# Performance work log

Hardware: AMD Instinct MI355X
Metric: run time of the kernel (lower is better)

The kernel has to match this reference:

```python
import jax, jax.numpy as jnp
import numpy as np

N = 512
H = 128
L = 4
NUM_RBF = 50
CUTOFF = 5.0
NMOL = 16
OUT = 1


def setup_inputs() -> dict:
    key = jax.random.key(0)
    ks = jax.random.split(key, 12)
    s = lambda f: 1.0 / np.sqrt(f)
    atomic_numbers = jax.random.randint(ks[0], (N,), 0, 100)
    positions = jax.random.normal(ks[1], (N, 3), dtype=jnp.float32) * 2.0
    batch = jnp.sort(jax.random.randint(ks[2], (N,), 0, NMOL))
    return {
        'atomic_numbers': atomic_numbers,
        'positions': positions,
        'batch': batch,
        'embed': jax.random.normal(ks[3], (100, H), dtype=jnp.float32) * 0.1,
        'msg_w1': jax.random.normal(ks[4], (L, H + NUM_RBF + 3, H), dtype=jnp.float32) * s(H + NUM_RBF + 3),
        'msg_b1': jnp.zeros((L, H), jnp.float32),
        'msg_w2': jax.random.normal(ks[5], (L, H, H), dtype=jnp.float32) * s(H),
        'msg_b2': jnp.zeros((L, H), jnp.float32),
        'upd_w1': jax.random.normal(ks[6], (L, 2 * H, H), dtype=jnp.float32) * s(2 * H),
        'upd_b1': jnp.zeros((L, H), jnp.float32),
        'upd_w2': jax.random.normal(ks[7], (L, H, H), dtype=jnp.float32) * s(H),
        'upd_b2': jnp.zeros((L, H), jnp.float32),
        'out_w1': jax.random.normal(ks[8], (H, H // 2), dtype=jnp.float32) * s(H),
        'out_b1': jnp.zeros((H // 2,), jnp.float32),
        'out_w2': jax.random.normal(ks[9], (H // 2, OUT), dtype=jnp.float32) * s(H // 2),
        'out_b2': jnp.zeros((OUT,), jnp.float32),
    }


def _forward(atomic_numbers, positions, batch, embed, msg_w1, msg_b1, msg_w2,
             msg_b2, upd_w1, upd_b1, upd_w2, upd_b2, out_w1, out_b1, out_w2, out_b2):
    x = embed[jnp.clip(atomic_numbers, 0, 99)]                      # [N,H]
    # all-pairs geometry: row i = source, col j = target (matches repeat_interleave/repeat)
    diff = positions[:, None, :] - positions[None, :, :]            # [N,N,3]
    dist = jnp.linalg.norm(diff, axis=-1)                           # [N,N]
    not_self = jnp.arange(N)[:, None] != jnp.arange(N)[None, :]
    valid = (dist < CUTOFF) & not_self                              # [N,N] edge mask
    dirs = diff / jnp.maximum(dist, 1e-8)[..., None]                # [N,N,3]
    # gaussian RBF: centers linspace(0, cutoff, num_rbf), width = cutoff/num_rbf
    centers = jnp.linspace(0.0, CUTOFF, NUM_RBF)
    width = CUTOFF / NUM_RBF
    rbf = jnp.exp(-(dist[..., None] - centers) ** 2 / (2.0 * width ** 2))  # [N,N,50]

    for l in range(L):
        # Linear over concat([x_j, rbf, dirs]) split by input blocks (same math)
        Wx = msg_w1[l, :H]
        Wr = msg_w1[l, H:H + NUM_RBF]
        Wd = msg_w1[l, H + NUM_RBF:]
        pre = (x @ Wx)[:, None, :] \
            + jnp.einsum('ijr,rh->ijh', rbf, Wr) \
            + jnp.einsum('ijd,dh->ijh', dirs, Wd) + msg_b1[l]       # [N,N,H]
        m = jax.nn.silu(pre) @ msg_w2[l] + msg_b2[l]                # [N,N,H]
        m = jnp.where(valid[..., None], m, 0.0)
        aggr = m.sum(axis=0)                                        # scatter-add to target j
        upd_in = jnp.concatenate([x, aggr], axis=-1)                # [N,2H]
        x = x + jax.nn.silu(upd_in @ upd_w1[l] + upd_b1[l]) @ upd_w2[l] + upd_b2[l]

    # per-molecule mean pool
    sums = jax.ops.segment_sum(x, batch, num_segments=NMOL)         # [NMOL,H]
    counts = jax.ops.segment_sum(jnp.ones((N,), x.dtype), batch, num_segments=NMOL)
    pooled = sums / jnp.maximum(counts, 1.0)[:, None]
    return jax.nn.silu(pooled @ out_w1 + out_b1) @ out_w2 + out_b2  # [NMOL,OUT]


def reference(atomic_numbers, positions, batch, embed, msg_w1, msg_b1, msg_w2,
              msg_b2, upd_w1, upd_b1, upd_w2, upd_b2, out_w1, out_b1, out_w2, out_b2):
    return _forward(atomic_numbers, positions, batch, embed, msg_w1, msg_b1, msg_w2,
                    msg_b2, upd_w1, upd_b1, upd_w2, upd_b2, out_w1, out_b1, out_w2, out_b2)
```

## Files before the change

### kernel.cpp

```cpp
#include <hip/hip_runtime.h>
#include <math.h>

#define N 512
#define H 128
#define L 4
#define NUM_RBF 50
#define NMOL 16
#define SUPER 64
#define MAXS 8

typedef __attribute__((ext_vector_type(8))) short short8;
typedef __attribute__((ext_vector_type(4))) float float4v;
typedef __attribute__((ext_vector_type(4))) int int4v;

__device__ __forceinline__ float silu_f(float v) {
    return v / (1.0f + __expf(-v));
}

__device__ __forceinline__ unsigned short f2bf(float f) {
    unsigned int u = __float_as_uint(f);
    unsigned int r = (u + 0x7FFFu + ((u >> 16) & 1u)) >> 16;
    return (unsigned short)r;
}

__device__ __forceinline__ void gld_lds16(const void* g, void* l) {
    __builtin_amdgcn_global_load_lds(
        (const __attribute__((address_space(1))) unsigned int*)g,
        (__attribute__((address_space(3))) unsigned int*)l, 16, 0, 0);
}

__global__ __launch_bounds__(512) void k_embed_lin(const int* __restrict__ an,
                                                   const float* __restrict__ embed,
                                                   const float* __restrict__ pos,
                                                   const float* __restrict__ wx,
                                                   const float* __restrict__ b1,
                                                   float* __restrict__ x,
                                                   float* __restrict__ a,
                                                   int* __restrict__ nbr,
                                                   int* __restrict__ ncnt,
                                                   unsigned short* __restrict__ Fg) {
    int j = blockIdx.x;
    int tid = threadIdx.x;
    int lane = tid & 63;
    int wave = tid >> 6;
    int h = tid & 127;
    int grp = tid >> 7;

    __shared__ float xs[H];
    __shared__ int wsum8[8];
    __shared__ float part[4][H];

    float pjx = pos[j * 3 + 0], pjy = pos[j * 3 + 1], pjz = pos[j * 3 + 2];

    if (tid < H) {
        int z = an[j];
        z = min(max(z, 0), 99);
        float xv = embed[z * H + tid];
        xs[tid] = xv;
        x[j * H + tid] = xv;
    }

    int padded;
    {
        int i = tid;
        float dx = pos[i * 3 + 0] - pjx;
        float dy = pos[i * 3 + 1] - pjy;
        float dz = pos[i * 3 + 2] - pjz;
        float d2 = dx * dx + dy * dy + dz * dz;
        int valid = (d2 < 25.0f) && (i != j);
        unsigned long long m = __ballot(valid);
        int pre = __popcll(m & ((1ull << lane) - 1ull));
        if (lane == 0) wsum8[wave] = __popcll(m);
        __syncthreads();
        int wbase = 0, total = 0;
        for (int w = 0; w < 8; w++) {
            if (w < wave) wbase += wsum8[w];
            total += wsum8[w];
        }
        if (valid) nbr[j * 512 + wbase + pre] = i;
        padded = (total + 63) & ~63;
        for (int s = total + tid; s < padded; s += 512) nbr[j * 512 + s] = j;
        if (tid == 0) ncnt[j] = total;
    }

    {
        float p0 = 0.f, p1 = 0.f, p2 = 0.f, p3 = 0.f;
        int k0 = grp * 32;
#pragma unroll 8
        for (int k = 0; k < 32; k += 4) {
            p0 += xs[k0 + k]     * wx[(k0 + k)     * H + h];
            p1 += xs[k0 + k + 1] * wx[(k0 + k + 1) * H + h];
            p2 += xs[k0 + k + 2] * wx[(k0 + k + 2) * H + h];
            p3 += xs[k0 + k + 3] * wx[(k0 + k + 3) * H + h];
        }
        part[grp][h] = (p0 + p1) + (p2 + p3);
    }
    __syncthreads();
    if (grp == 0)
        a[j * H + h] = part[0][h] + part[1][h] + part[2][h] + part[3][h] + b1[h];

    const float DELTA = 5.0f / 49.0f;
    int kb = (tid & 3) * 16;
#pragma unroll
    for (int pass = 0; pass < 4; pass++) {
        int slot = pass * 128 + (tid >> 2);
        if (slot < padded) {
            int ni = nbr[j * 512 + slot];
            float dx = pos[ni * 3 + 0] - pjx;
            float dy = pos[ni * 3 + 1] - pjy;
            float dz = pos[ni * 3 + 2] - pjz;
            float d = sqrtf(dx * dx + dy * dy + dz * dz);
            float rinv = 1.0f / fmaxf(d, 1e-8f);
            unsigned short vals[16];
#pragma unroll
            for (int qq = 0; qq < 16; qq++) {
                int k = kb + qq;
                float v;
                if (k < NUM_RBF) {
                    float tt = d - (float)k * DELTA;
                    v = __expf(-50.0f * tt * tt);
                } else if (k == NUM_RBF)     v = dx * rinv;
                else if (k == NUM_RBF + 1)   v = dy * rinv;
                else if (k == NUM_RBF + 2)   v = dz * rinv;
                else                         v = 0.0f;
                vals[qq] = f2bf(v);
            }
            int row = slot & 63;
            unsigned short* tile = Fg + (((size_t)(j * MAXS + (slot >> 6))) << 12);
            int c0 = kb >> 3;
            int4v p0, p1;
#pragma unroll
            for (int q = 0; q < 4; q++) {
                p0[q] = (int)((unsigned)vals[2 * q]     | ((unsigned)vals[2 * q + 1] << 16));
                p1[q] = (int)((unsigned)vals[8 + 2 * q] | ((unsigned)vals[9 + 2 * q] << 16));
            }
            *(int4v*)(tile + row * 64 + (((c0    ) ^ (row & 7)) << 3)) = p0;
            *(int4v*)(tile + row * 64 + (((c0 + 1) ^ (row & 7)) << 3)) = p1;
        }
    }
}

__global__ __launch_bounds__(512) void k_layer(const float* __restrict__ a,
                                               const int* __restrict__ nbr,
                                               const int* __restrict__ ncnt,
                                               const unsigned short* __restrict__ Fg,
                                               const float* __restrict__ wfeat,
                                               const float* __restrict__ w2,
                                               const float* __restrict__ b2,
                                               const float* __restrict__ u1,
                                               const float* __restrict__ ub1,
                                               const float* __restrict__ u2,
                                               const float* __restrict__ ub2,
                                               float* __restrict__ x,
                                               const float* __restrict__ wxn,
                                               const float* __restrict__ b1n,
                                               float* __restrict__ a_next) {
    int j = blockIdx.x;
    int tid = threadIdx.x;
    int g = tid >> 8;
    int lane = tid & 63;
    int wv4 = (tid >> 6) & 3;
    int nn = lane & 15;
    int quad = lane >> 4;
    int hbase = wv4 * 32;

    __shared__ __align__(16) unsigned short F[2][2][SUPER * 64];
    __shared__ __align__(16) int nidx_all[512];
    __shared__ float sjp[2][H];
    __shared__ float sj[H], xj[H], ag[H], hid[H], xn[H];
    __shared__ float part[4][H];

    int cnt = ncnt[j];

    if (tid < 2 * H) sjp[tid >> 7][tid & 127] = 0.0f;
    if (tid < H) xj[tid] = x[j * H + tid];
    nidx_all[tid] = nbr[j * 512 + tid];

    short8 bfrag[2][2];
    for (int c = 0; c < 2; c++) {
        for (int t = 0; t < 2; t++) {
            short8 b;
            int h = hbase + 16 * t + nn;
#pragma unroll
            for (int jj = 0; jj < 8; jj++) {
                int k = c * 32 + quad * 8 + jj;
                float v = (k < NUM_RBF + 3) ? wfeat[k * H + h] : 0.0f;
                b[jj] = (short)f2bf(v);
            }
            bfrag[c][t] = b;
        }
    }

    int S = (cnt + 63) >> 6;
    int rounds = (S + 1) >> 1;

    auto stage_tile = [&](int s, int b) {
        const char* src = (const char*)(Fg + (((size_t)(j * MAXS + s)) << 12));
        char* dst = (char*)&F[g][b][0];
#pragma unroll
        for (int q = 0; q < 2; q++) {
            int off = (wv4 + 4 * q) << 10;
            gld_lds16(src + off + lane * 16, dst + off);
        }
    };

    if (g < S) stage_tile(g, 0);
    __syncthreads();

    float pacc0 = 0.0f, pacc1 = 0.0f;

    for (int r = 0; r < rounds; r++) {
        int s = 2 * r + g;
        int sn = 2 * (r + 1) + g;
        if (sn < S) stage_tile(sn, (r + 1) & 1);
        if (s < S) {
            int cur = r & 1;
#pragma unroll
            for (int it = 0; it < SUPER / 16; it++) {
                int lbase = it * 16 + quad * 4;
                int4v ni4 = *(const int4v*)&nidx_all[s * 64 + lbase];
                float av0[4], av1[4];
#pragma unroll
                for (int rr = 0; rr < 4; rr++) {
                    av0[rr] = a[ni4[rr] * H + hbase + nn];
                    av1[rr] = a[ni4[rr] * H + hbase + 16 + nn];
                }
                int row = it * 16 + nn;
                const char* fb = (const char*)&F[g][cur][0] + row * 128;
                short8 afrag0 = *(const short8*)(fb + ((quad       ^ (row & 7)) << 4));
                short8 afrag1 = *(const short8*)(fb + (((quad + 4) ^ (row & 7)) << 4));
                float4v acc0 = {0.0f, 0.0f, 0.0f, 0.0f};
                float4v acc1 = {0.0f, 0.0f, 0.0f, 0.0f};
                acc0 = __builtin_amdgcn_mfma_f32_16x16x32_bf16(afrag0, bfrag[0][0], acc0, 0, 0, 0);
                acc0 = __builtin_amdgcn_mfma_f32_16x16x32_bf16(afrag1, bfrag[1][0], acc0, 0, 0, 0);
                acc1 = __builtin_amdgcn_mfma_f32_16x16x32_bf16(afrag0, bfrag[0][1], acc1, 0, 0, 0);
                acc1 = __builtin_amdgcn_mfma_f32_16x16x32_bf16(afrag1, bfrag[1][1], acc1, 0, 0, 0);
#pragma unroll
                for (int rr = 0; rr < 4; rr++) {
                    float vm = (s * 64 + lbase + rr < cnt) ? 1.0f : 0.0f;
                    pacc0 += vm * silu_f(acc0[rr] + av0[rr]);
                    pacc1 += vm * silu_f(acc1[rr] + av1[rr]);
                }
            }
        }
        __syncthreads();
    }

    pacc0 += __shfl_xor(pacc0, 16, 64);
    pacc0 += __shfl_xor(pacc0, 32, 64);
    pacc1 += __shfl_xor(pacc1, 16, 64);
    pacc1 += __shfl_xor(pacc1, 32, 64);
    if (lane < 16) {
        sjp[g][hbase + lane]      = pacc0;
        sjp[g][hbase + 16 + lane] = pacc1;
    }
    __syncthreads();
    if (tid < H) sj[tid] = sjp[0][tid] + sjp[1][tid];
    __syncthreads();

    int h = tid & 127;
    int grp = tid >> 7;

    {
        float p0 = 0.f, p1 = 0.f, p2 = 0.f, p3 = 0.f;
        int k0 = grp * 32;
#pragma unroll 8
        for (int k = 0; k < 32; k += 4) {
            p0 += sj[k0 + k]     * w2[(k0 + k)     * H + h];
            p1 += sj[k0 + k + 1] * w2[(k0 + k + 1) * H + h];
            p2 += sj[k0 + k + 2] * w2[(k0 + k + 2) * H + h];
            p3 += sj[k0 + k + 3] * w2[(k0 + k + 3) * H + h];
        }
        part[grp][h] = (p0 + p1) + (p2 + p3);
    }
    __syncthreads();
    if (grp == 0) ag[h] = part[0][h] + part[1][h] + part[2][h] + part[3][h] + (float)cnt * b2[h];
    __syncthreads();

    {
        const float* src = (grp < 2) ? xj : ag;
        int sbase = (grp & 1) * 64;
        int k0 = grp * 64;
        float p0 = 0.f, p1 = 0.f, p2 = 0.f, p3 = 0.f;
#pragma unroll 8
        for (int k = 0; k < 64; k += 4) {
            p0 += src[sbase + k]     * u1[(k0 + k)     * H + h];
            p1 += src[sbase + k + 1] * u1[(k0 + k + 1) * H + h];
            p2 += src[sbase + k + 2] * u1[(k0 + k + 2) * H + h];
            p3 += src[sbase + k + 3] * u1[(k0 + k + 3) * H + h];
        }
        part[grp][h] = (p0 + p1) + (p2 + p3);
    }
    __syncthreads();
    if (grp == 0) hid[h] = silu_f(part[0][h] + part[1][h] + part[2][h] + part[3][h] + ub1[h]);
    __syncthreads();

    {
        float p0 = 0.f, p1 = 0.f, p2 = 0.f, p3 = 0.f;
        int k0 = grp * 32;
#pragma unroll 8
        for (int k = 0; k < 32; k += 4) {
            p0 += hid[k0 + k]     * u2[(k0 + k)     * H + h];
            p1 += hid[k0 + k + 1] * u2[(k0 + k + 1) * H + h];
            p2 += hid[k0 + k + 2] * u2[(k0 + k + 2) * H + h];
            p3 += hid[k0 + k + 3] * u2[(k0 + k + 3) * H + h];
        }
        part[grp][h] = (p0 + p1) + (p2 + p3);
    }
    __syncthreads();
    if (grp == 0) {
        float xv = xj[h] + part[0][h] + part[1][h] + part[2][h] + part[3][h] + ub2[h];
        x[j * H + h] = xv;
        xn[h] = xv;
    }

    if (a_next != nullptr) {
        __syncthreads();
        float p0 = 0.f, p1 = 0.f, p2 = 0.f, p3 = 0.f;
        int k0 = grp * 32;
#pragma unroll 8
        for (int k = 0; k < 32; k += 4) {
            p0 += xn[k0 + k]     * wxn[(k0 + k)     * H + h];
            p1 += xn[k0 + k + 1] * wxn[(k0 + k + 1) * H + h];
            p2 += xn[k0 + k + 2] * wxn[(k0 + k + 2) * H + h];
            p3 += xn[k0 + k + 3] * wxn[(k0 + k + 3) * H + h];
        }
        part[grp][h] = (p0 + p1) + (p2 + p3);
        __syncthreads();
        if (grp == 0)
            a_next[j * H + h] = part[0][h] + part[1][h] + part[2][h] + part[3][h] + b1n[h];
    }
}

__global__ __launch_bounds__(512) void k_pool(const float* __restrict__ x,
                                              const int* __restrict__ batch,
                                              const float* __restrict__ ow1,
                                              const float* __restrict__ ob1,
                                              const float* __restrict__ ow2,
                                              const float* __restrict__ ob2,
                                              float* __restrict__ out) {
    int m = blockIdx.x;
    int tid = threadIdx.x;
    int h = tid & 127;
    int q = tid >> 7;
    __shared__ int lo_s, hi_s;
    __shared__ float psum[4][H];
    __shared__ float pooled[H];
    __shared__ float hid[H / 2];

    if (tid == 0) {
        int a = 0, b = N;
        while (a < b) { int mid = (a + b) >> 1; if (batch[mid] < m) a = mid + 1; else b = mid; }
        lo_s = a;
        b = N;
        while (a < b) { int mid = (a + b) >> 1; if (batch[mid] < m + 1) a = mid + 1; else b = mid; }
        hi_s = a;
    }
    __syncthreads();

    int lo = lo_s, hi = hi_s;
    float s = 0.0f;
    for (int i = lo + q; i < hi; i += 4) s += x[i * H + h];
    psum[q][h] = s;
    __syncthreads();
    if (q == 0) pooled[h] = (psum[0][h] + psum[1][h] + psum[2][h] + psum[3][h]) / (float)max(hi - lo, 1);
    __syncthreads();

    if (tid < H / 2) {
        float p0 = 0.f, p1 = 0.f;
        for (int k = 0; k < H; k += 2) {
            p0 += pooled[k]     * ow1[(k)     * (H / 2) + h];
            p1 += pooled[k + 1] * ow1[(k + 1) * (H / 2) + h];
        }
        hid[h] = silu_f(p0 + p1 + ob1[h]);
    }
    __syncthreads();

    if (tid == 0) {
        float o = ob2[0];
        for (int k = 0; k < H / 2; k++) o += hid[k] * ow2[k];
        out[m] = o;
    }
}

extern "C" void kernel_launch(void* const* d_in, const int* in_sizes, int n_in,
                              void* d_out, int out_size, void* d_ws, size_t ws_size,
                              hipStream_t stream) {
    const int*   an      = (const int*)d_in[0];
    const float* pos     = (const float*)d_in[1];
    const int*   batch   = (const int*)d_in[2];
    const float* embed   = (const float*)d_in[3];
    const float* msg_w1  = (const float*)d_in[4];
    const float* msg_b1  = (const float*)d_in[5];
    const float* msg_w2  = (const float*)d_in[6];
    const float* msg_b2  = (const float*)d_in[7];
    const float* upd_w1  = (const float*)d_in[8];
    const float* upd_b1  = (const float*)d_in[9];
    const float* upd_w2  = (const float*)d_in[10];
    const float* upd_b2  = (const float*)d_in[11];
    const float* out_w1  = (const float*)d_in[12];
    const float* out_b1  = (const float*)d_in[13];
    const float* out_w2  = (const float*)d_in[14];
    const float* out_b2  = (const float*)d_in[15];
    float* out = (float*)d_out;

    float* x    = (float*)d_ws;
    float* a0   = x + N * H;
    float* a1   = a0 + N * H;
    int*   nbr  = (int*)(a1 + N * H);
    int*   ncnt = nbr + N * 512;
    unsigned short* Fg = (unsigned short*)(ncnt + N);

    const int W1ROWS = H + NUM_RBF + 3;

    k_embed_lin<<<N, 512, 0, stream>>>(an, embed, pos, msg_w1, msg_b1, x, a0, nbr, ncnt, Fg);
    for (int l = 0; l < L; l++) {
        float* a_cur  = (l & 1) ? a1 : a0;
        float* a_next = (l + 1 < L) ? ((l & 1) ? a0 : a1) : nullptr;
        const float* wxn = (l + 1 < L) ? (msg_w1 + (l + 1) * W1ROWS * H) : nullptr;
        const float* b1n = (l + 1 < L) ? (msg_b1 + (l + 1) * H) : nullptr;
        k_layer<<<N, 512, 0, stream>>>(a_cur, nbr, ncnt, Fg,
                                       msg_w1 + l * W1ROWS * H + H * H,
                                       msg_w2 + l * H * H, msg_b2 + l * H,
                                       upd_w1 + l * 2 * H * H, upd_b1 + l * H,
                                       upd_w2 + l * H * H, upd_b2 + l * H,
                                       x, wxn, b1n, a_next);
    }
    k_pool<<<NMOL, 512, 0, stream>>>(x, batch, out_w1, out_b1, out_w2, out_b2, out);
}
```

Measured before the change: 215.8 us.

## Split layer kernel into message and batched 4-node update kernels

The fused per-node layer kernel is split into k_msg, which computes each node's summed message activation and writes it to a global buffer, and k_upd, which runs the dense update MLP for four nodes per block. In k_upd each weight load is reused across four rows, and the per-block partial-sum reductions with their extra barriers go away. In exchange each layer now launches twice and makes an extra global round trip for the intermediate sums, and the update kernel runs only 128 blocks.

```diff
diff --git a/kernel.cpp b/kernel.cpp
--- a/kernel.cpp
+++ b/kernel.cpp
@@ -140,21 +140,12 @@
     }
 }
 
-__global__ __launch_bounds__(512) void k_layer(const float* __restrict__ a,
-                                               const int* __restrict__ nbr,
-                                               const int* __restrict__ ncnt,
-                                               const unsigned short* __restrict__ Fg,
-                                               const float* __restrict__ wfeat,
-                                               const float* __restrict__ w2,
-                                               const float* __restrict__ b2,
-                                               const float* __restrict__ u1,
-                                               const float* __restrict__ ub1,
-                                               const float* __restrict__ u2,
-                                               const float* __restrict__ ub2,
-                                               float* __restrict__ x,
-                                               const float* __restrict__ wxn,
-                                               const float* __restrict__ b1n,
-                                               float* __restrict__ a_next) {
+__global__ __launch_bounds__(512) void k_msg(const float* __restrict__ a,
+                                             const int* __restrict__ nbr,
+                                             const int* __restrict__ ncnt,
+                                             const unsigned short* __restrict__ Fg,
+                                             const float* __restrict__ wfeat,
+                                             float* __restrict__ sjg) {
     int j = blockIdx.x;
     int tid = threadIdx.x;
     int g = tid >> 8;
@@ -167,13 +158,8 @@
     __shared__ __align__(16) unsigned short F[2][2][SUPER * 64];
     __shared__ __align__(16) int nidx_all[512];
     __shared__ float sjp[2][H];
-    __shared__ float sj[H], xj[H], ag[H], hid[H], xn[H];
-    __shared__ float part[4][H];
 
     int cnt = ncnt[j];
-
-    if (tid < 2 * H) sjp[tid >> 7][tid & 127] = 0.0f;
-    if (tid < H) xj[tid] = x[j * H + tid];
     nidx_all[tid] = nbr[j * 512 + tid];
 
     short8 bfrag[2][2];
@@ -255,80 +241,92 @@
         sjp[g][hbase + 16 + lane] = pacc1;
     }
     __syncthreads();
-    if (tid < H) sj[tid] = sjp[0][tid] + sjp[1][tid];
-    __syncthreads();
-
+    if (tid < H) sjg[j * H + tid] = sjp[0][tid] + sjp[1][tid];
+}
+
+__global__ __launch_bounds__(512) void k_upd(const float* __restrict__ sjg,
+                                             const int* __restrict__ ncnt,
+                                             const float* __restrict__ w2,
+                                             const float* __restrict__ b2,
+                                             const float* __restrict__ u1,
+                                             const float* __restrict__ ub1,
+                                             const float* __restrict__ u2,
+                                             const float* __restrict__ ub2,
+                                             float* __restrict__ x,
+                                             const float* __restrict__ wxn,
+                                             const float* __restrict__ b1n,
+                                             float* __restrict__ a_next) {
+    int j0 = blockIdx.x * 4;
+    int tid = threadIdx.x;
     int h = tid & 127;
-    int grp = tid >> 7;
+    int r = tid >> 7;
+
+    __shared__ float sj[4][H], xj[4][H], ag[4][H], hid[4][H], xn[4][H];
+    __shared__ float cntv[4];
+
+    sj[r][h] = sjg[(j0 + r) * H + h];
+    xj[r][h] = x[(j0 + r) * H + h];
+    if (tid < 4) cntv[tid] = (float)ncnt[j0 + tid];
+    __syncthreads();
 
     {
         float p0 = 0.f, p1 = 0.f, p2 = 0.f, p3 = 0.f;
-        int k0 = grp * 32;
-#pragma unroll 8
-        for (int k = 0; k < 32; k += 4) {
-            p0 += sj[k0 + k]     * w2[(k0 + k)     * H + h];
-            p1 += sj[k0 + k + 1] * w2[(k0 + k + 1) * H + h];
-            p2 += sj[k0 + k + 2] * w2[(k0 + k + 2) * H + h];
-            p3 += sj[k0 + k + 3] * w2[(k0 + k + 3) * H + h];
-        }
-        part[grp][h] = (p0 + p1) + (p2 + p3);
-    }
-    __syncthreads();
-    if (grp == 0) ag[h] = part[0][h] + part[1][h] + part[2][h] + part[3][h] + (float)cnt * b2[h];
-    __syncthreads();
-
-    {
-        const float* src = (grp < 2) ? xj : ag;
-        int sbase = (grp & 1) * 64;
-        int k0 = grp * 64;
-        float p0 = 0.f, p1 = 0.f, p2 = 0.f, p3 = 0.f;
-#pragma unroll 8
-        for (int k = 0; k < 64; k += 4) {
-            p0 += src[sbase + k]     * u1[(k0 + k)     * H + h];
-            p1 += src[sbase + k + 1] * u1[(k0 + k + 1) * H + h];
-            p2 += src[sbase + k + 2] * u1[(k0 + k + 2) * H + h];
-            p3 += src[sbase + k + 3] * u1[(k0 + k + 3) * H + h];
-        }
-        part[grp][h] = (p0 + p1) + (p2 + p3);
-    }
-    __syncthreads();
-    if (grp == 0) hid[h] = silu_f(part[0][h] + part[1][h] + part[2][h] + part[3][h] + ub1[h]);
+#pragma unroll 8
+        for (int k = 0; k < H; k += 4) {
+            p0 += sj[r][k]     * w2[(k)     * H + h];
+            p1 += sj[r][k + 1] * w2[(k + 1) * H + h];
+            p2 += sj[r][k + 2] * w2[(k + 2) * H + h];
+            p3 += sj[r][k + 3] * w2[(k + 3) * H + h];
+        }
+        ag[r][h] = (p0 + p1) + (p2 + p3) + cntv[r] * b2[h];
+    }
     __syncthreads();
 
     {
         float p0 = 0.f, p1 = 0.f, p2 = 0.f, p3 = 0.f;
-        int k0 = grp * 32;
-#pragma unroll 8
-        for (int k = 0; k < 32; k += 4) {
-            p0 += hid[k0 + k]     * u2[(k0 + k)     * H + h];
-            p1 += hid[k0 + k + 1] * u2[(k0 + k + 1) * H + h];
-            p2 += hid[k0 + k + 2] * u2[(k0 + k + 2) * H + h];
-            p3 += hid[k0 + k + 3] * u2[(k0 + k + 3) * H + h];
-        }
-        part[grp][h] = (p0 + p1) + (p2 + p3);
-    }
-    __syncthreads();
-    if (grp == 0) {
-        float xv = xj[h] + part[0][h] + part[1][h] + part[2][h] + part[3][h] + ub2[h];
-        x[j * H + h] = xv;
-        xn[h] = xv;
+#pragma unroll 8
+        for (int k = 0; k < H; k += 4) {
+            p0 += xj[r][k]     * u1[(k)     * H + h];
+            p1 += xj[r][k + 1] * u1[(k + 1) * H + h];
+            p2 += xj[r][k + 2] * u1[(k + 2) * H + h];
+            p3 += xj[r][k + 3] * u1[(k + 3) * H + h];
+        }
+#pragma unroll 8
+        for (int k = 0; k < H; k += 4) {
+            p0 += ag[r][k]     * u1[(H + k)     * H + h];
+            p1 += ag[r][k + 1] * u1[(H + k + 1) * H + h];
+            p2 += ag[r][k + 2] * u1[(H + k + 2) * H + h];
+            p3 += ag[r][k + 3] * u1[(H + k + 3) * H + h];
+        }
+        hid[r][h] = silu_f((p0 + p1) + (p2 + p3) + ub1[h]);
+    }
+    __syncthreads();
+
+    {
+        float p0 = 0.f, p1 = 0.f, p2 = 0.f, p3 = 0.f;
+#pragma unroll 8
+        for (int k = 0; k < H; k += 4) {
+            p0 += hid[r][k]     * u2[(k)     * H + h];
+            p1 += hid[r][k + 1] * u2[(k + 1) * H + h];
+            p2 += hid[r][k + 2] * u2[(k + 2) * H + h];
+            p3 += hid[r][k + 3] * u2[(k + 3) * H + h];
+        }
+        float xv = xj[r][h] + (p0 + p1) + (p2 + p3) + ub2[h];
+        x[(j0 + r) * H + h] = xv;
+        xn[r][h] = xv;
     }
 
     if (a_next != nullptr) {
         __syncthreads();
         float p0 = 0.f, p1 = 0.f, p2 = 0.f, p3 = 0.f;
-        int k0 = grp * 32;
-#pragma unroll 8
-        for (int k = 0; k < 32; k += 4) {
-            p0 += xn[k0 + k]     * wxn[(k0 + k)     * H + h];
-            p1 += xn[k0 + k + 1] * wxn[(k0 + k + 1) * H + h];
-            p2 += xn[k0 + k + 2] * wxn[(k0 + k + 2) * H + h];
-            p3 += xn[k0 + k + 3] * wxn[(k0 + k + 3) * H + h];
-        }
-        part[grp][h] = (p0 + p1) + (p2 + p3);
-        __syncthreads();
-        if (grp == 0)
-            a_next[j * H + h] = part[0][h] + part[1][h] + part[2][h] + part[3][h] + b1n[h];
+#pragma unroll 8
+        for (int k = 0; k < H; k += 4) {
+            p0 += xn[r][k]     * wxn[(k)     * H + h];
+            p1 += xn[r][k + 1] * wxn[(k + 1) * H + h];
+            p2 += xn[r][k + 2] * wxn[(k + 2) * H + h];
+            p3 += xn[r][k + 3] * wxn[(k + 3) * H + h];
+        }
+        a_next[(j0 + r) * H + h] = (p0 + p1) + (p2 + p3) + b1n[h];
     }
 }
 
@@ -407,7 +405,8 @@
     float* x    = (float*)d_ws;
     float* a0   = x + N * H;
     float* a1   = a0 + N * H;
-    int*   nbr  = (int*)(a1 + N * H);
+    float* sjg  = a1 + N * H;
+    int*   nbr  = (int*)(sjg + N * H);
     int*   ncnt = nbr + N * 512;
     unsigned short* Fg = (unsigned short*)(ncnt + N);
 
@@ -419,12 +418,13 @@
         float* a_next = (l + 1 < L) ? ((l & 1) ? a0 : a1) : nullptr;
         const float* wxn = (l + 1 < L) ? (msg_w1 + (l + 1) * W1ROWS * H) : nullptr;
         const float* b1n = (l + 1 < L) ? (msg_b1 + (l + 1) * H) : nullptr;
-        k_layer<<<N, 512, 0, stream>>>(a_cur, nbr, ncnt, Fg,
-                                       msg_w1 + l * W1ROWS * H + H * H,
-                                       msg_w2 + l * H * H, msg_b2 + l * H,
-                                       upd_w1 + l * 2 * H * H, upd_b1 + l * H,
-                                       upd_w2 + l * H * H, upd_b2 + l * H,
-                                       x, wxn, b1n, a_next);
+        k_msg<<<N, 512, 0, stream>>>(a_cur, nbr, ncnt, Fg,
+                                     msg_w1 + l * W1ROWS * H + H * H, sjg);
+        k_upd<<<N / 4, 512, 0, stream>>>(sjg, ncnt,
+                                         msg_w2 + l * H * H, msg_b2 + l * H,
+                                         upd_w1 + l * 2 * H * H, upd_b1 + l * H,
+                                         upd_w2 + l * H * H, upd_b2 + l * H,
+                                         x, wxn, b1n, a_next);
     }
     k_pool<<<NMOL, 512, 0, stream>>>(x, batch, out_w1, out_b1, out_w2, out_b2, out);
 }
```

Result: slower. 245.5 us (+13.8%).

## Fuse all layers into one persistent cooperative kernel with grid syncs

Applied to the files above, without the earlier changes.

Replaces the six separate launches (embed, four layers, pool) with a single cooperative kernel of 256 blocks. Each block owns two nodes for the whole run and keeps their x state, neighbour lists and counts in shared memory. Layers are separated by grid.sync(), which removes per-launch overhead and the global round-trips for x, nbr and ncnt. In exchange, each block does twice the serial work with half the blocks, and every layer waits on a grid-wide barrier.

```diff
diff --git a/kernel.cpp b/kernel.cpp
--- a/kernel.cpp
+++ b/kernel.cpp
@@ -1,5 +1,8 @@
 #include <hip/hip_runtime.h>
+#include <hip/hip_cooperative_groups.h>
 #include <math.h>
+
+namespace cg = cooperative_groups;
 
 #define N 512
 #define H 128
@@ -8,6 +11,7 @@
 #define NMOL 16
 #define SUPER 64
 #define MAXS 8
+#define NB 256
 
 typedef __attribute__((ext_vector_type(8))) short short8;
 typedef __attribute__((ext_vector_type(4))) float float4v;
@@ -29,363 +33,357 @@
         (__attribute__((address_space(3))) unsigned int*)l, 16, 0, 0);
 }
 
-__global__ __launch_bounds__(512) void k_embed_lin(const int* __restrict__ an,
-                                                   const float* __restrict__ embed,
-                                                   const float* __restrict__ pos,
-                                                   const float* __restrict__ wx,
-                                                   const float* __restrict__ b1,
-                                                   float* __restrict__ x,
-                                                   float* __restrict__ a,
-                                                   int* __restrict__ nbr,
-                                                   int* __restrict__ ncnt,
-                                                   unsigned short* __restrict__ Fg) {
-    int j = blockIdx.x;
-    int tid = threadIdx.x;
-    int lane = tid & 63;
-    int wave = tid >> 6;
-    int h = tid & 127;
-    int grp = tid >> 7;
-
-    __shared__ float xs[H];
+__global__ __launch_bounds__(512) void k_all(
+    const int* __restrict__ an, const float* __restrict__ pos,
+    const int* __restrict__ batch, const float* __restrict__ embed,
+    const float* __restrict__ msg_w1, const float* __restrict__ msg_b1,
+    const float* __restrict__ msg_w2, const float* __restrict__ msg_b2,
+    const float* __restrict__ upd_w1, const float* __restrict__ upd_b1,
+    const float* __restrict__ upd_w2, const float* __restrict__ upd_b2,
+    const float* __restrict__ ow1, const float* __restrict__ ob1,
+    const float* __restrict__ ow2, const float* __restrict__ ob2,
+    float* __restrict__ out,
+    float* __restrict__ xg, float* __restrict__ a0g, float* __restrict__ a1g,
+    unsigned short* __restrict__ Fg)
+{
+    cg::grid_group grid = cg::this_grid();
+    const int bid = blockIdx.x;
+    const int tid = threadIdx.x;
+    const int lane = tid & 63;
+    const int wave = tid >> 6;
+    const int h128 = tid & 127;
+    const int grp = tid >> 7;
+    const int g = tid >> 8;
+    const int wv4 = (tid >> 6) & 3;
+    const int nn = lane & 15;
+    const int quad = lane >> 4;
+    const int hbase = wv4 * 32;
+
+    __shared__ __align__(16) unsigned short F[2][2][SUPER * 64];
+    __shared__ __align__(16) int nidx[2][512];
+    __shared__ float xcur[2][H];
+    __shared__ float sjv[2][H], sjp[2][H];
+    __shared__ float tp[4][H];
+    __shared__ float agv[2][H], hidv[2][H];
     __shared__ int wsum8[8];
-    __shared__ float part[4][H];
-
-    float pjx = pos[j * 3 + 0], pjy = pos[j * 3 + 1], pjz = pos[j * 3 + 2];
-
-    if (tid < H) {
-        int z = an[j];
-        z = min(max(z, 0), 99);
-        float xv = embed[z * H + tid];
-        xs[tid] = xv;
-        x[j * H + tid] = xv;
+    __shared__ int cnt_s[2];
+    __shared__ int lo_s, hi_s;
+
+    for (int n = 0; n < 2; n++) {
+        const int j = bid + n * NB;
+        const float pjx = pos[j * 3 + 0], pjy = pos[j * 3 + 1], pjz = pos[j * 3 + 2];
+
+        if (tid < H) {
+            int z = an[j];
+            z = min(max(z, 0), 99);
+            xcur[n][tid] = embed[z * H + tid];
+        }
+
+        int padded;
+        {
+            int i = tid;
+            float dx = pos[i * 3 + 0] - pjx;
+            float dy = pos[i * 3 + 1] - pjy;
+            float dz = pos[i * 3 + 2] - pjz;
+            float d2 = dx * dx + dy * dy + dz * dz;
+            int valid = (d2 < 25.0f) && (i != j);
+            unsigned long long m = __ballot(valid);
+            int pre = __popcll(m & ((1ull << lane) - 1ull));
+            if (lane == 0) wsum8[wave] = __popcll(m);
+            __syncthreads();
+            int wbase = 0, total = 0;
+            for (int w = 0; w < 8; w++) {
+                if (w < wave) wbase += wsum8[w];
+                total += wsum8[w];
+            }
+            if (valid) nidx[n][wbase + pre] = i;
+            padded = (total + 63) & ~63;
+            for (int s = total + tid; s < padded; s += 512) nidx[n][s] = j;
+            if (tid == 0) cnt_s[n] = total;
+        }
+
+        {
+            float p0 = 0.f, p1 = 0.f, p2 = 0.f, p3 = 0.f;
+            int k0 = grp * 32;
+#pragma unroll 8
+            for (int k = 0; k < 32; k += 4) {
+                p0 += xcur[n][k0 + k]     * msg_w1[(k0 + k)     * H + h128];
+                p1 += xcur[n][k0 + k + 1] * msg_w1[(k0 + k + 1) * H + h128];
+                p2 += xcur[n][k0 + k + 2] * msg_w1[(k0 + k + 2) * H + h128];
+                p3 += xcur[n][k0 + k + 3] * msg_w1[(k0 + k + 3) * H + h128];
+            }
+            tp[grp][h128] = (p0 + p1) + (p2 + p3);
+        }
+        __syncthreads();
+        if (grp == 0)
+            a0g[j * H + h128] = tp[0][h128] + tp[1][h128] + tp[2][h128] + tp[3][h128] + msg_b1[h128];
+
+        {
+            const float DELTA = 5.0f / 49.0f;
+            int kb = (tid & 3) * 16;
+#pragma unroll
+            for (int pass = 0; pass < 4; pass++) {
+                int slot = pass * 128 + (tid >> 2);
+                if (slot < padded) {
+                    int ni = nidx[n][slot];
+                    float dx = pos[ni * 3 + 0] - pjx;
+                    float dy = pos[ni * 3 + 1] - pjy;
+                    float dz = pos[ni * 3 + 2] - pjz;
+                    float d = sqrtf(dx * dx + dy * dy + dz * dz);
+                    float rinv = 1.0f / fmaxf(d, 1e-8f);
+                    unsigned short vals[16];
+#pragma unroll
+                    for (int qq = 0; qq < 16; qq++) {
+                        int k = kb + qq;
+                        float v;
+                        if (k < NUM_RBF) {
+                            float tt = d - (float)k * DELTA;
+                            v = __expf(-50.0f * tt * tt);
+                        } else if (k == NUM_RBF)     v = dx * rinv;
+                        else if (k == NUM_RBF + 1)   v = dy * rinv;
+                        else if (k == NUM_RBF + 2)   v = dz * rinv;
+                        else                         v = 0.0f;
+                        vals[qq] = f2bf(v);
+                    }
+                    int row = slot & 63;
+                    unsigned short* tile = Fg + (((size_t)(j * MAXS + (slot >> 6))) << 12);
+                    int c0 = kb >> 3;
+                    int4v p0, p1;
+#pragma unroll
+                    for (int q = 0; q < 4; q++) {
+                        p0[q] = (int)((unsigned)vals[2 * q]     | ((unsigned)vals[2 * q + 1] << 16));
+                        p1[q] = (int)((unsigned)vals[8 + 2 * q] | ((unsigned)vals[9 + 2 * q] << 16));
+                    }
+                    *(int4v*)(tile + row * 64 + (((c0    ) ^ (row & 7)) << 3)) = p0;
+                    *(int4v*)(tile + row * 64 + (((c0 + 1) ^ (row & 7)) << 3)) = p1;
+                }
+            }
+        }
+        __syncthreads();
     }
-
-    int padded;
-    {
-        int i = tid;
-        float dx = pos[i * 3 + 0] - pjx;
-        float dy = pos[i * 3 + 1] - pjy;
-        float dz = pos[i * 3 + 2] - pjz;
-        float d2 = dx * dx + dy * dy + dz * dz;
-        int valid = (d2 < 25.0f) && (i != j);
-        unsigned long long m = __ballot(valid);
-        int pre = __popcll(m & ((1ull << lane) - 1ull));
-        if (lane == 0) wsum8[wave] = __popcll(m);
-        __syncthreads();
-        int wbase = 0, total = 0;
-        for (int w = 0; w < 8; w++) {
-            if (w < wave) wbase += wsum8[w];
-            total += wsum8[w];
-        }
-        if (valid) nbr[j * 512 + wbase + pre] = i;
-        padded = (total + 63) & ~63;
-        for (int s = total + tid; s < padded; s += 512) nbr[j * 512 + s] = j;
-        if (tid == 0) ncnt[j] = total;
+    grid.sync();
+
+    const int W1R = H + NUM_RBF + 3;
+    for (int l = 0; l < L; l++) {
+        const float* wfeat = msg_w1 + l * W1R * H + H * H;
+        const float* w2  = msg_w2 + l * H * H;
+        const float* b2  = msg_b2 + l * H;
+        const float* u1  = upd_w1 + l * 2 * H * H;
+        const float* ub1 = upd_b1 + l * H;
+        const float* u2  = upd_w2 + l * H * H;
+        const float* ub2 = upd_b2 + l * H;
+        const float* acur = (l & 1) ? a1g : a0g;
+        float* anext = (l & 1) ? a0g : a1g;
+        const float* wxn = msg_w1 + (l + 1) * W1R * H;
+        const float* b1n = msg_b1 + (l + 1) * H;
+
+        short8 bfrag[2][2];
+        for (int c = 0; c < 2; c++) {
+            for (int t = 0; t < 2; t++) {
+                short8 b;
+                int hh = hbase + 16 * t + nn;
+#pragma unroll
+                for (int jj = 0; jj < 8; jj++) {
+                    int k = c * 32 + quad * 8 + jj;
+                    float v = (k < NUM_RBF + 3) ? wfeat[k * H + hh] : 0.0f;
+                    b[jj] = (short)f2bf(v);
+                }
+                bfrag[c][t] = b;
+            }
+        }
+
+        for (int n = 0; n < 2; n++) {
+            const int j = bid + n * NB;
+            int cnt = cnt_s[n];
+            int S = (cnt + 63) >> 6;
+            int rounds = (S + 1) >> 1;
+
+            auto stage_tile = [&](int s, int b) {
+                const char* src = (const char*)(Fg + (((size_t)(j * MAXS + s)) << 12));
+                char* dst = (char*)&F[g][b][0];
+#pragma unroll
+                for (int q = 0; q < 2; q++) {
+                    int off = (wv4 + 4 * q) << 10;
+                    gld_lds16(src + off + lane * 16, dst + off);
+                }
+            };
+
+            if (g < S) stage_tile(g, 0);
+            __syncthreads();
+
+            float pacc0 = 0.0f, pacc1 = 0.0f;
+            for (int r = 0; r < rounds; r++) {
+                int s = 2 * r + g;
+                int sn = 2 * (r + 1) + g;
+                if (sn < S) stage_tile(sn, (r + 1) & 1);
+                if (s < S) {
+                    int cur = r & 1;
+#pragma unroll
+                    for (int it = 0; it < SUPER / 16; it++) {
+                        int lbase = it * 16 + quad * 4;
+                        int4v ni4 = *(const int4v*)&nidx[n][s * 64 + lbase];
+                        float av0[4], av1[4];
+#pragma unroll
+                        for (int rr = 0; rr < 4; rr++) {
+                            av0[rr] = acur[ni4[rr] * H + hbase + nn];
+                            av1[rr] = acur[ni4[rr] * H + hbase + 16 + nn];
+                        }
+                        int row = it * 16 + nn;
+                        const char* fb = (const char*)&F[g][cur][0] + row * 128;
+                        short8 af0 = *(const short8*)(fb + ((quad       ^ (row & 7)) << 4));
+                        short8 af1 = *(const short8*)(fb + (((quad + 4) ^ (row & 7)) << 4));
+                        float4v acc0 = {0.0f, 0.0f, 0.0f, 0.0f};
+                        float4v acc1 = {0.0f, 0.0f, 0.0f, 0.0f};
+                        acc0 = __builtin_amdgcn_mfma_f32_16x16x32_bf16(af0, bfrag[0][0], acc0, 0, 0, 0);
+                        acc0 = __builtin_amdgcn_mfma_f32_16x16x32_bf16(af1, bfrag[1][0], acc0, 0, 0, 0);
+                        acc1 = __builtin_amdgcn_mfma_f32_16x16x32_bf16(af0, bfrag[0][1], acc1, 0, 0, 0);
+                        acc1 = __builtin_amdgcn_mfma_f32_16x16x32_bf16(af1, bfrag[1][1], acc1, 0, 0, 0);
+#pragma unroll
+                        for (int rr = 0; rr < 4; rr++) {
+                            float vm = (s * 64 + lbase + rr < cnt) ? 1.0f : 0.0f;
+                            pacc0 += vm * silu_f(acc0[rr] + av0[rr]);
+                            pacc1 += vm * silu_f(acc1[rr] + av1[rr]);
+                        }
+                    }
+                }
+                __syncthreads();
+            }
+
+            pacc0 += __shfl_xor(pacc0, 16, 64);
+            pacc0 += __shfl_xor(pacc0, 32, 64);
+            pacc1 += __shfl_xor(pacc1, 16, 64);
+            pacc1 += __shfl_xor(pacc1, 32, 64);
+            if (lane < 16) {
+                sjp[g][hbase + lane]      = pacc0;
+                sjp[g][hbase + 16 + lane] = pacc1;
+            }
+            __syncthreads();
+            if (tid < H) sjv[n][tid] = sjp[0][tid] + sjp[1][tid];
+            __syncthreads();
+        }
+
+        {
+            int node = tid >> 8;
+            int kh = (tid >> 7) & 1;
+            int h = tid & 127;
+            int ti = node * 2 + kh;
+            int j = bid + node * NB;
+
+            {
+                int k0 = kh * 64;
+                float p0 = 0.f, p1 = 0.f, p2 = 0.f, p3 = 0.f;
+#pragma unroll 8
+                for (int k = 0; k < 64; k += 4) {
+                    p0 += sjv[node][k0 + k]     * w2[(k0 + k)     * H + h];
+                    p1 += sjv[node][k0 + k + 1] * w2[(k0 + k + 1) * H + h];
+                    p2 += sjv[node][k0 + k + 2] * w2[(k0 + k + 2) * H + h];
+                    p3 += sjv[node][k0 + k + 3] * w2[(k0 + k + 3) * H + h];
+                }
+                tp[ti][h] = (p0 + p1) + (p2 + p3);
+            }
+            __syncthreads();
+            if (kh == 0)
+                agv[node][h] = tp[node * 2][h] + tp[node * 2 + 1][h] + (float)cnt_s[node] * b2[h];
+            __syncthreads();
+
+            {
+                float p0 = 0.f, p1 = 0.f, p2 = 0.f, p3 = 0.f;
+                const float* src = (kh == 0) ? &xcur[node][0] : &agv[node][0];
+                const float* w = (kh == 0) ? u1 : (u1 + H * H);
+#pragma unroll 8
+                for (int k = 0; k < H; k += 4) {
+                    p0 += src[k]     * w[(k)     * H + h];
+                    p1 += src[k + 1] * w[(k + 1) * H + h];
+                    p2 += src[k + 2] * w[(k + 2) * H + h];
+                    p3 += src[k + 3] * w[(k + 3) * H + h];
+                }
+                tp[ti][h] = (p0 + p1) + (p2 + p3);
+            }
+            __syncthreads();
+            if (kh == 0)
+                hidv[node][h] = silu_f(tp[node * 2][h] + tp[node * 2 + 1][h] + ub1[h]);
+            __syncthreads();
+
+            {
+                int k0 = kh * 64;
+                float p0 = 0.f, p1 = 0.f, p2 = 0.f, p3 = 0.f;
+#pragma unroll 8
+                for (int k = 0; k < 64; k += 4) {
+                    p0 += hidv[node][k0 + k]     * u2[(k0 + k)     * H + h];
+                    p1 += hidv[node][k0 + k + 1] * u2[(k0 + k + 1) * H + h];
+                    p2 += hidv[node][k0 + k + 2] * u2[(k0 + k + 2) * H + h];
+                    p3 += hidv[node][k0 + k + 3] * u2[(k0 + k + 3) * H + h];
+                }
+                tp[ti][h] = (p0 + p1) + (p2 + p3);
+            }
+            __syncthreads();
+            if (kh == 0) {
+                float xv = xcur[node][h] + tp[node * 2][h] + tp[node * 2 + 1][h] + ub2[h];
+                xcur[node][h] = xv;
+                if (l == L - 1) xg[j * H + h] = xv;
+            }
+            __syncthreads();
+
+            if (l < L - 1) {
+                int k0 = kh * 64;
+                float p0 = 0.f, p1 = 0.f, p2 = 0.f, p3 = 0.f;
+#pragma unroll 8
+                for (int k = 0; k < 64; k += 4) {
+                    p0 += xcur[node][k0 + k]     * wxn[(k0 + k)     * H + h];
+                    p1 += xcur[node][k0 + k + 1] * wxn[(k0 + k + 1) * H + h];
+                    p2 += xcur[node][k0 + k + 2] * wxn[(k0 + k + 2) * H + h];
+                    p3 += xcur[node][k0 + k + 3] * wxn[(k0 + k + 3) * H + h];
+                }
+                tp[ti][h] = (p0 + p1) + (p2 + p3);
+                __syncthreads();
+                if (kh == 0)
+                    anext[j * H + h] = tp[node * 2][h] + tp[node * 2 + 1][h] + b1n[h];
+            }
+        }
+        grid.sync();
     }
 
-    {
-        float p0 = 0.f, p1 = 0.f, p2 = 0.f, p3 = 0.f;
-        int k0 = grp * 32;
-#pragma unroll 8
-        for (int k = 0; k < 32; k += 4) {
-            p0 += xs[k0 + k]     * wx[(k0 + k)     * H + h];
-            p1 += xs[k0 + k + 1] * wx[(k0 + k + 1) * H + h];
-            p2 += xs[k0 + k + 2] * wx[(k0 + k + 2) * H + h];
-            p3 += xs[k0 + k + 3] * wx[(k0 + k + 3) * H + h];
-        }
-        part[grp][h] = (p0 + p1) + (p2 + p3);
-    }
-    __syncthreads();
-    if (grp == 0)
-        a[j * H + h] = part[0][h] + part[1][h] + part[2][h] + part[3][h] + b1[h];
-
-    const float DELTA = 5.0f / 49.0f;
-    int kb = (tid & 3) * 16;
-#pragma unroll
-    for (int pass = 0; pass < 4; pass++) {
-        int slot = pass * 128 + (tid >> 2);
-        if (slot < padded) {
-            int ni = nbr[j * 512 + slot];
-            float dx = pos[ni * 3 + 0] - pjx;
-            float dy = pos[ni * 3 + 1] - pjy;
-            float dz = pos[ni * 3 + 2] - pjz;
-            float d = sqrtf(dx * dx + dy * dy + dz * dz);
-            float rinv = 1.0f / fmaxf(d, 1e-8f);
-            unsigned short vals[16];
-#pragma unroll
-            for (int qq = 0; qq < 16; qq++) {
-                int k = kb + qq;
-                float v;
-                if (k < NUM_RBF) {
-                    float tt = d - (float)k * DELTA;
-                    v = __expf(-50.0f * tt * tt);
-                } else if (k == NUM_RBF)     v = dx * rinv;
-                else if (k == NUM_RBF + 1)   v = dy * rinv;
-                else if (k == NUM_RBF + 2)   v = dz * rinv;
-                else                         v = 0.0f;
-                vals[qq] = f2bf(v);
-            }
-            int row = slot & 63;
-            unsigned short* tile = Fg + (((size_t)(j * MAXS + (slot >> 6))) << 12);
-            int c0 = kb >> 3;
-            int4v p0, p1;
-#pragma unroll
-            for (int q = 0; q < 4; q++) {
-                p0[q] = (int)((unsigned)vals[2 * q]     | ((unsigned)vals[2 * q + 1] << 16));
-                p1[q] = (int)((unsigned)vals[8 + 2 * q] | ((unsigned)vals[9 + 2 * q] << 16));
-            }
-            *(int4v*)(tile + row * 64 + (((c0    ) ^ (row & 7)) << 3)) = p0;
-            *(int4v*)(tile + row * 64 + (((c0 + 1) ^ (row & 7)) << 3)) = p1;
-        }
-    }
-}
-
-__global__ __launch_bounds__(512) void k_layer(const float* __restrict__ a,
-                                               const int* __restrict__ nbr,
-                                               const int* __restrict__ ncnt,
-                                               const unsigned short* __restrict__ Fg,
-                                               const float* __restrict__ wfeat,
-                                               const float* __restrict__ w2,
-                                               const float* __restrict__ b2,
-                                               const float* __restrict__ u1,
-                                               const float* __restrict__ ub1,
-                                               const float* __restrict__ u2,
-                                               const float* __restrict__ ub2,
-                                               float* __restrict__ x,
-                                               const float* __restrict__ wxn,
-                                               const float* __restrict__ b1n,
-                                               float* __restrict__ a_next) {
-    int j = blockIdx.x;
-    int tid = threadIdx.x;
-    int g = tid >> 8;
-    int lane = tid & 63;
-    int wv4 = (tid >> 6) & 3;
-    int nn = lane & 15;
-    int quad = lane >> 4;
-    int hbase = wv4 * 32;
-
-    __shared__ __align__(16) unsigned short F[2][2][SUPER * 64];
-    __shared__ __align__(16) int nidx_all[512];
-    __shared__ float sjp[2][H];
-    __shared__ float sj[H], xj[H], ag[H], hid[H], xn[H];
-    __shared__ float part[4][H];
-
-    int cnt = ncnt[j];
-
-    if (tid < 2 * H) sjp[tid >> 7][tid & 127] = 0.0f;
-    if (tid < H) xj[tid] = x[j * H + tid];
-    nidx_all[tid] = nbr[j * 512 + tid];
-
-    short8 bfrag[2][2];
-    for (int c = 0; c < 2; c++) {
-        for (int t = 0; t < 2; t++) {
-            short8 b;
-            int h = hbase + 16 * t + nn;
-#pragma unroll
-            for (int jj = 0; jj < 8; jj++) {
-                int k = c * 32 + quad * 8 + jj;
-                float v = (k < NUM_RBF + 3) ? wfeat[k * H + h] : 0.0f;
-                b[jj] = (short)f2bf(v);
-            }
-            bfrag[c][t] = b;
-        }
-    }
-
-    int S = (cnt + 63) >> 6;
-    int rounds = (S + 1) >> 1;
-
-    auto stage_tile = [&](int s, int b) {
-        const char* src = (const char*)(Fg + (((size_t)(j * MAXS + s)) << 12));
-        char* dst = (char*)&F[g][b][0];
-#pragma unroll
-        for (int q = 0; q < 2; q++) {
-            int off = (wv4 + 4 * q) << 10;
-            gld_lds16(src + off + lane * 16, dst + off);
-        }
-    };
-
-    if (g < S) stage_tile(g, 0);
-    __syncthreads();
-
-    float pacc0 = 0.0f, pacc1 = 0.0f;
-
-    for (int r = 0; r < rounds; r++) {
-        int s = 2 * r + g;
-        int sn = 2 * (r + 1) + g;
-        if (sn < S) stage_tile(sn, (r + 1) & 1);
-        if (s < S) {
-            int cur = r & 1;
-#pragma unroll
-            for (int it = 0; it < SUPER / 16; it++) {
-                int lbase = it * 16 + quad * 4;
-                int4v ni4 = *(const int4v*)&nidx_all[s * 64 + lbase];
-                float av0[4], av1[4];
-#pragma unroll
-                for (int rr = 0; rr < 4; rr++) {
-                    av0[rr] = a[ni4[rr] * H + hbase + nn];
-                    av1[rr] = a[ni4[rr] * H + hbase + 16 + nn];
-                }
-                int row = it * 16 + nn;
-                const char* fb = (const char*)&F[g][cur][0] + row * 128;
-                short8 afrag0 = *(const short8*)(fb + ((quad       ^ (row & 7)) << 4));
-                short8 afrag1 = *(const short8*)(fb + (((quad + 4) ^ (row & 7)) << 4));
-                float4v acc0 = {0.0f, 0.0f, 0.0f, 0.0f};
-                float4v acc1 = {0.0f, 0.0f, 0.0f, 0.0f};
-                acc0 = __builtin_amdgcn_mfma_f32_16x16x32_bf16(afrag0, bfrag[0][0], acc0, 0, 0, 0);
-                acc0 = __builtin_amdgcn_mfma_f32_16x16x32_bf16(afrag1, bfrag[1][0], acc0, 0, 0, 0);
-                acc1 = __builtin_amdgcn_mfma_f32_16x16x32_bf16(afrag0, bfrag[0][1], acc1, 0, 0, 0);
-                acc1 = __builtin_amdgcn_mfma_f32_16x16x32_bf16(afrag1, bfrag[1][1], acc1, 0, 0, 0);
-#pragma unroll
-                for (int rr = 0; rr < 4; rr++) {
-                    float vm = (s * 64 + lbase + rr < cnt) ? 1.0f : 0.0f;
-                    pacc0 += vm * silu_f(acc0[rr] + av0[rr]);
-                    pacc1 += vm * silu_f(acc1[rr] + av1[rr]);
-                }
-            }
-        }
-        __syncthreads();
-    }
-
-    pacc0 += __shfl_xor(pacc0, 16, 64);
-    pacc0 += __shfl_xor(pacc0, 32, 64);
-    pacc1 += __shfl_xor(pacc1, 16, 64);
-    pacc1 += __shfl_xor(pacc1, 32, 64);
-    if (lane < 16) {
-        sjp[g][hbase + lane]      = pacc0;
-        sjp[g][hbase + 16 + lane] = pacc1;
-    }
-    __syncthreads();
-    if (tid < H) sj[tid] = sjp[0][tid] + sjp[1][tid];
-    __syncthreads();
-
-    int h = tid & 127;
-    int grp = tid >> 7;
-
-    {
-        float p0 = 0.f, p1 = 0.f, p2 = 0.f, p3 = 0.f;
-        int k0 = grp * 32;
-#pragma unroll 8
-        for (int k = 0; k < 32; k += 4) {
-            p0 += sj[k0 + k]     * w2[(k0 + k)     * H + h];
-            p1 += sj[k0 + k + 1] * w2[(k0 + k + 1) * H + h];
-            p2 += sj[k0 + k + 2] * w2[(k0 + k + 2) * H + h];
-            p3 += sj[k0 + k + 3] * w2[(k0 + k + 3) * H + h];
-        }
-        part[grp][h] = (p0 + p1) + (p2 + p3);
-    }
-    __syncthreads();
-    if (grp == 0) ag[h] = part[0][h] + part[1][h] + part[2][h] + part[3][h] + (float)cnt * b2[h];
-    __syncthreads();
-
-    {
-        const float* src = (grp < 2) ? xj : ag;
-        int sbase = (grp & 1) * 64;
-        int k0 = grp * 64;
-        float p0 = 0.f, p1 = 0.f, p2 = 0.f, p3 = 0.f;
-#pragma unroll 8
-        for (int k = 0; k < 64; k += 4) {
-            p0 += src[sbase + k]     * u1[(k0 + k)     * H + h];
-            p1 += src[sbase + k + 1] * u1[(k0 + k + 1) * H + h];
-            p2 += src[sbase + k + 2] * u1[(k0 + k + 2) * H + h];
-            p3 += src[sbase + k + 3] * u1[(k0 + k + 3) * H + h];
-        }
-        part[grp][h] = (p0 + p1) + (p2 + p3);
-    }
-    __syncthreads();
-    if (grp == 0) hid[h] = silu_f(part[0][h] + part[1][h] + part[2][h] + part[3][h] + ub1[h]);
-    __syncthreads();
-
-    {
-        float p0 = 0.f, p1 = 0.f, p2 = 0.f, p3 = 0.f;
-        int k0 = grp * 32;
-#pragma unroll 8
-        for (int k = 0; k < 32; k += 4) {
-            p0 += hid[k0 + k]     * u2[(k0 + k)     * H + h];
-            p1 += hid[k0 + k + 1] * u2[(k0 + k + 1) * H + h];
-            p2 += hid[k0 + k + 2] * u2[(k0 + k + 2) * H + h];
-            p3 += hid[k0 + k + 3] * u2[(k0 + k + 3) * H + h];
-        }
-        part[grp][h] = (p0 + p1) + (p2 + p3);
-    }
-    __syncthreads();
-    if (grp == 0) {
-        float xv = xj[h] + part[0][h] + part[1][h] + part[2][h] + part[3][h] + ub2[h];
-        x[j * H + h] = xv;
-        xn[h] = xv;
-    }
-
-    if (a_next != nullptr) {
-        __syncthreads();
-        float p0 = 0.f, p1 = 0.f, p2 = 0.f, p3 = 0.f;
-        int k0 = grp * 32;
-#pragma unroll 8
-        for (int k = 0; k < 32; k += 4) {
-            p0 += xn[k0 + k]     * wxn[(k0 + k)     * H + h];
-            p1 += xn[k0 + k + 1] * wxn[(k0 + k + 1) * H + h];
-            p2 += xn[k0 + k + 2] * wxn[(k0 + k + 2) * H + h];
-            p3 += xn[k0 + k + 3] * wxn[(k0 + k + 3) * H + h];
-        }
-        part[grp][h] = (p0 + p1) + (p2 + p3);
-        __syncthreads();
-        if (grp == 0)
-            a_next[j * H + h] = part[0][h] + part[1][h] + part[2][h] + part[3][h] + b1n[h];
-    }
-}
-
-__global__ __launch_bounds__(512) void k_pool(const float* __restrict__ x,
-                                              const int* __restrict__ batch,
-                                              const float* __restrict__ ow1,
-                                              const float* __restrict__ ob1,
-                                              const float* __restrict__ ow2,
-                                              const float* __restrict__ ob2,
-                                              float* __restrict__ out) {
-    int m = blockIdx.x;
-    int tid = threadIdx.x;
-    int h = tid & 127;
-    int q = tid >> 7;
-    __shared__ int lo_s, hi_s;
-    __shared__ float psum[4][H];
-    __shared__ float pooled[H];
-    __shared__ float hid[H / 2];
-
-    if (tid == 0) {
-        int a = 0, b = N;
-        while (a < b) { int mid = (a + b) >> 1; if (batch[mid] < m) a = mid + 1; else b = mid; }
-        lo_s = a;
-        b = N;
-        while (a < b) { int mid = (a + b) >> 1; if (batch[mid] < m + 1) a = mid + 1; else b = mid; }
-        hi_s = a;
-    }
-    __syncthreads();
-
-    int lo = lo_s, hi = hi_s;
-    float s = 0.0f;
-    for (int i = lo + q; i < hi; i += 4) s += x[i * H + h];
-    psum[q][h] = s;
-    __syncthreads();
-    if (q == 0) pooled[h] = (psum[0][h] + psum[1][h] + psum[2][h] + psum[3][h]) / (float)max(hi - lo, 1);
-    __syncthreads();
-
-    if (tid < H / 2) {
-        float p0 = 0.f, p1 = 0.f;
-        for (int k = 0; k < H; k += 2) {
-            p0 += pooled[k]     * ow1[(k)     * (H / 2) + h];
-            p1 += pooled[k + 1] * ow1[(k + 1) * (H / 2) + h];
-        }
-        hid[h] = silu_f(p0 + p1 + ob1[h]);
-    }
-    __syncthreads();
-
-    if (tid == 0) {
-        float o = ob2[0];
-        for (int k = 0; k < H / 2; k++) o += hid[k] * ow2[k];
-        out[m] = o;
+    if (bid < NMOL) {
+        int m = bid;
+        int q = tid >> 7, h = tid & 127;
+        if (tid == 0) {
+            int a = 0, b = N;
+            while (a < b) { int mid = (a + b) >> 1; if (batch[mid] < m) a = mid + 1; else b = mid; }
+            lo_s = a;
+            b = N;
+            while (a < b) { int mid = (a + b) >> 1; if (batch[mid] < m + 1) a = mid + 1; else b = mid; }
+            hi_s = a;
+        }
+        __syncthreads();
+        int lo = lo_s, hi = hi_s;
+        float s = 0.0f;
+        for (int i = lo + q; i < hi; i += 4) s += xg[i * H + h];
+        tp[q][h] = s;
+        __syncthreads();
+        if (q == 0)
+            sjv[0][h] = (tp[0][h] + tp[1][h] + tp[2][h] + tp[3][h]) / (float)max(hi - lo, 1);
+        __syncthreads();
+        if (tid < H / 2) {
+            float p0 = 0.f, p1 = 0.f;
+            for (int k = 0; k < H; k += 2) {
+                p0 += sjv[0][k]     * ow1[(k)     * (H / 2) + tid];
+                p1 += sjv[0][k + 1] * ow1[(k + 1) * (H / 2) + tid];
+            }
+            hidv[0][tid] = silu_f(p0 + p1 + ob1[tid]);
+        }
+        __syncthreads();
+        if (tid == 0) {
+            float o = ob2[0];
+            for (int k = 0; k < H / 2; k++) o += hidv[0][k] * ow2[k];
+            out[m] = o;
+        }
     }
 }
 
 extern "C" void kernel_launch(void* const* d_in, const int* in_sizes, int n_in,
                               void* d_out, int out_size, void* d_ws, size_t ws_size,
                               hipStream_t stream) {
+    (void)in_sizes; (void)n_in; (void)out_size; (void)ws_size;
     const int*   an      = (const int*)d_in[0];
     const float* pos     = (const float*)d_in[1];
     const int*   batch   = (const int*)d_in[2];
@@ -404,27 +402,17 @@
     const float* out_b2  = (const float*)d_in[15];
     float* out = (float*)d_out;
 
-    float* x    = (float*)d_ws;
-    float* a0   = x + N * H;
-    float* a1   = a0 + N * H;
-    int*   nbr  = (int*)(a1 + N * H);
-    int*   ncnt = nbr + N * 512;
-    unsigned short* Fg = (unsigned short*)(ncnt + N);
-
-    const int W1ROWS = H + NUM_RBF + 3;
-
-    k_embed_lin<<<N, 512, 0, stream>>>(an, embed, pos, msg_w1, msg_b1, x, a0, nbr, ncnt, Fg);
-    for (int l = 0; l < L; l++) {
-        float* a_cur  = (l & 1) ? a1 : a0;
-        float* a_next = (l + 1 < L) ? ((l & 1) ? a0 : a1) : nullptr;
-        const float* wxn = (l + 1 < L) ? (msg_w1 + (l + 1) * W1ROWS * H) : nullptr;
-        const float* b1n = (l + 1 < L) ? (msg_b1 + (l + 1) * H) : nullptr;
-        k_layer<<<N, 512, 0, stream>>>(a_cur, nbr, ncnt, Fg,
-                                       msg_w1 + l * W1ROWS * H + H * H,
-                                       msg_w2 + l * H * H, msg_b2 + l * H,
-                                       upd_w1 + l * 2 * H * H, upd_b1 + l * H,
-                                       upd_w2 + l * H * H, upd_b2 + l * H,
-                                       x, wxn, b1n, a_next);
-    }
-    k_pool<<<NMOL, 512, 0, stream>>>(x, batch, out_w1, out_b1, out_w2, out_b2, out);
+    float* xg  = (float*)d_ws;
+    float* a0g = xg + N * H;
+    float* a1g = a0g + N * H;
+    unsigned short* Fg = (unsigned short*)(a1g + N * H);
+
+    void* args[] = {
+        (void*)&an, (void*)&pos, (void*)&batch, (void*)&embed,
+        (void*)&msg_w1, (void*)&msg_b1, (void*)&msg_w2, (void*)&msg_b2,
+        (void*)&upd_w1, (void*)&upd_b1, (void*)&upd_w2, (void*)&upd_b2,
+        (void*)&out_w1, (void*)&out_b1, (void*)&out_w2, (void*)&out_b2,
+        (void*)&out, (void*)&xg, (void*)&a0g, (void*)&a1g, (void*)&Fg
+    };
+    hipLaunchCooperativeKernel((const void*)k_all, dim3(NB), dim3(512), args, 0u, stream);
 }
```

Measured after the change: 424.5 us. 1.97x slower.
